# Performance work log

Hardware: AMD Instinct MI355X
Metric: run time of the kernel (lower is better)

The kernel has to match this reference:

```python
import jax, jax.numpy as jnp
import numpy as np
import math

B, S, IN = 16, 512, 8
D, H, L, FF, OUT = 512, 8, 4, 2048, 1
VAR_DIM = D // IN  # 64, even -> only sin/cos even-dim path in the original loop
HD = D // H
EPS = 1e-5


def setup_inputs() -> dict:
    key = jax.random.key(0)
    ks = jax.random.split(key, 20)
    s = 0.02
    inp = {
        "features": jax.random.normal(ks[0], (B, S, IN), dtype=jnp.float32),
        "position_indices": jax.random.randint(ks[1], (B, S), 0, 512, dtype=jnp.int64 if jax.config.jax_enable_x64 else jnp.int32),
        "w_in": jax.random.normal(ks[2], (IN, D), dtype=jnp.float32) * s,
        "b_in": jnp.zeros((D,), jnp.float32),
        "qkv_w": jax.random.normal(ks[3], (L, D, 3 * D), dtype=jnp.float32) * s,
        "qkv_b": jnp.zeros((L, 3 * D), jnp.float32),
        "attn_out_w": jax.random.normal(ks[4], (L, D, D), dtype=jnp.float32) * s,
        "attn_out_b": jnp.zeros((L, D), jnp.float32),
        "ln1_g": jnp.ones((L, D), jnp.float32),
        "ln1_b": jnp.zeros((L, D), jnp.float32),
        "ff1_w": jax.random.normal(ks[5], (L, D, FF), dtype=jnp.float32) * s,
        "ff1_b": jnp.zeros((L, FF), jnp.float32),
        "ff2_w": jax.random.normal(ks[6], (L, FF, D), dtype=jnp.float32) * s,
        "ff2_b": jnp.zeros((L, D), jnp.float32),
        "ln2_g": jnp.ones((L, D), jnp.float32),
        "ln2_b": jnp.zeros((L, D), jnp.float32),
        "w_out": jax.random.normal(ks[7], (D, OUT), dtype=jnp.float32) * s,
        "b_out": jnp.zeros((OUT,), jnp.float32),
    }
    return inp


def _pos_encoding(position_indices):
    # Vectorized replacement of the per-(b,i) Python loop.
    pos = position_indices.astype(jnp.float32)  # [B,S]
    div = jnp.exp(jnp.arange(0, VAR_DIM, 2, dtype=jnp.float32) * (-(math.log(10000.0) / VAR_DIM)))  # [VAR_DIM//2]
    ang = pos[:, :, None] * div  # [B,S,VAR_DIM//2]
    # interleave sin (even dims) / cos (odd dims) -> [B,S,VAR_DIM]
    block = jnp.stack([jnp.sin(ang), jnp.cos(ang)], axis=-1).reshape(pos.shape[0], pos.shape[1], VAR_DIM)
    # identical encoding per variable since var_positions == position_indices for all vars
    return jnp.tile(block, (1, 1, IN))  # [B,S,D]


def _layer_norm(x, g, b):
    mu = jnp.mean(x, axis=-1, keepdims=True)
    var = jnp.mean(jnp.square(x - mu), axis=-1, keepdims=True)
    return (x - mu) * jax.lax.rsqrt(var + EPS) * g + b


def _encoder_layer(x, qkv_w, qkv_b, ow, ob, g1, b1, f1w, f1b, f2w, f2b, g2, b2):
    Bx, Sx, _ = x.shape
    qkv = x @ qkv_w + qkv_b  # [B,S,3D]
    q, k, v = jnp.split(qkv, 3, axis=-1)
    q = q.reshape(Bx, Sx, H, HD)
    k = k.reshape(Bx, Sx, H, HD)
    v = v.reshape(Bx, Sx, H, HD)
    scores = jnp.einsum("bqhd,bkhd->bhqk", q, k) / math.sqrt(HD)
    attn = jax.nn.softmax(scores, axis=-1)
    ctx = jnp.einsum("bhqk,bkhd->bqhd", attn, v).reshape(Bx, Sx, D)
    attn_out = ctx @ ow + ob
    x = _layer_norm(x + attn_out, g1, b1)  # post-norm (PyTorch default norm_first=False)
    ff = jax.nn.relu(x @ f1w + f1b) @ f2w + f2b
    return _layer_norm(x + ff, g2, b2)


def reference(features, position_indices, w_in, b_in, qkv_w, qkv_b, attn_out_w, attn_out_b,
              ln1_g, ln1_b, ff1_w, ff1_b, ff2_w, ff2_b, ln2_g, ln2_b, w_out, b_out):
    x = features @ w_in + b_in  # input projection
    x = x + _pos_encoding(position_indices)
    for l in range(L):
        x = _encoder_layer(x, qkv_w[l], qkv_b[l], attn_out_w[l], attn_out_b[l],
                           ln1_g[l], ln1_b[l], ff1_w[l], ff1_b[l], ff2_w[l], ff2_b[l],
                           ln2_g[l], ln2_b[l])
    return x @ w_out + b_out  # [B,S,OUT]
```

## Files before the change

### kernel.cpp

```cpp
#include <hip/hip_runtime.h>
#include <cstdint>
#include <cstddef>

#define BATCH   16
#define SEQ     512
#define NTOK    8192
#define DMODEL  512
#define NHEAD   8
#define HDIM    64
#define FFDIM   2048
#define NLAYER  4

typedef unsigned short u16;
typedef __attribute__((ext_vector_type(8))) short bf16x8;
typedef __attribute__((ext_vector_type(8))) unsigned short us8;
typedef __attribute__((ext_vector_type(4))) float f32x4;

__device__ __forceinline__ float bf2f(u16 u) {
    union { float f; unsigned int i; } x; x.i = ((unsigned int)u) << 16; return x.f;
}
__device__ __forceinline__ u16 f2b(float f) {
    union { float f; unsigned int u; } a; a.f = f;
    unsigned int r = a.u + 0x7fff + ((a.u >> 16) & 1);
    return (u16)(r >> 16);
}

__device__ __forceinline__ void async_copy16(const void* g, void* l) {
    __builtin_amdgcn_global_load_lds(
        (const __attribute__((address_space(1))) unsigned int*)g,
        (__attribute__((address_space(3))) unsigned int*)l, 16, 0, 0);
}

__global__ __launch_bounds__(256) void embed_kernel(
    const float* __restrict__ feat, const int* __restrict__ pos,
    const float* __restrict__ w_in, const float* __restrict__ b_in,
    float* __restrict__ x, u16* __restrict__ xb)
{
    int idx = blockIdx.x * 256 + threadIdx.x;
    if (idx >= NTOK * DMODEL) return;
    int t = idx >> 9;
    int d = idx & 511;
    float acc = b_in[d];
#pragma unroll
    for (int i = 0; i < 8; ++i)
        acc += feat[t * 8 + i] * w_in[i * DMODEL + d];
    int p = pos[t];
    int dl = d & 63;
    int pair = dl >> 1;
    float div = expf(-(float)(2 * pair) * 0.14391156831212787f);
    float ang = (float)p * div;
    float pe = (dl & 1) ? cosf(ang) : sinf(ang);
    float v = acc + pe;
    x[idx] = v;
    xb[idx] = f2b(v);
}

__global__ __launch_bounds__(256) void transpose_w_kernel(
    const float* __restrict__ W, u16* __restrict__ WT, int K, int N)
{
    __shared__ float t[32][33];
    const float* Wl = W + (size_t)blockIdx.z * K * N;
    u16* WTl = WT + (size_t)blockIdx.z * K * N;
    int n0 = blockIdx.x * 32, k0 = blockIdx.y * 32;
    int c = threadIdx.x & 31, r8 = threadIdx.x >> 5;
#pragma unroll
    for (int i = 0; i < 4; ++i) {
        int r = r8 + i * 8;
        t[r][c] = Wl[(size_t)(k0 + r) * N + n0 + c];
    }
    __syncthreads();
#pragma unroll
    for (int i = 0; i < 4; ++i) {
        int r = r8 + i * 8;
        WTl[(size_t)(n0 + r) * K + k0 + c] = f2b(t[c][r]);
    }
}

template <int OUT_BF16, int RELU, int ADD_RESID>
__global__ __launch_bounds__(256) void gemm_bk64_kernel(
    const u16* __restrict__ A, const u16* __restrict__ BT,
    const float* __restrict__ bias, const float* __restrict__ resid,
    void* __restrict__ Cp, int M, int N, int K)
{
    __shared__ u16 As[128 * 64];
    __shared__ u16 Bs[128 * 64];
    const int tid = threadIdx.x;

    const int gx = gridDim.x, gy = gridDim.y;
    const int raw = blockIdx.x + gx * blockIdx.y;
    const int xcd = raw & 7;
    const int k8  = raw >> 3;
    const int ych = gy >> 3;
    const int m0 = (xcd * ych + k8 / gx) * 128;
    const int n0 = (k8 % gx) * 128;

    const int wid = tid >> 6, lane = tid & 63;
    const int wr = (wid >> 1) * 64, wc = (wid & 1) * 64;
    const int lr = lane & 15, lk16 = lane >> 4;
    const int sw = lr & 7;

    f32x4 acc[4][4] = {};

    for (int kt = 0; kt < K; kt += 64) {
        __syncthreads();
#pragma unroll
        for (int u = 0; u < 4; ++u) {
            int cc = u * 256 + tid;
            int row = cc >> 3, kc = cc & 7;
            async_copy16(&A[(size_t)(m0 + row) * K + kt + ((kc ^ (row & 7)) * 8)],
                         &As[cc * 8]);
        }
#pragma unroll
        for (int u = 0; u < 4; ++u) {
            int cc = u * 256 + tid;
            int row = cc >> 3, kc = cc & 7;
            async_copy16(&BT[(size_t)(n0 + row) * K + kt + ((kc ^ (row & 7)) * 8)],
                         &Bs[cc * 8]);
        }
        __syncthreads();

        bf16x8 a[4][2], b[4][2];
#pragma unroll
        for (int i = 0; i < 4; ++i)
#pragma unroll
            for (int kk = 0; kk < 2; ++kk) {
                a[i][kk] = *(const bf16x8*)&As[
                    (wr + i * 16 + lr) * 64 + (((kk * 4 + lk16) ^ sw) * 8)];
                b[i][kk] = *(const bf16x8*)&Bs[
                    (wc + i * 16 + lr) * 64 + (((kk * 4 + lk16) ^ sw) * 8)];
            }

        __builtin_amdgcn_s_setprio(1);
#pragma unroll
        for (int i = 0; i < 4; ++i)
#pragma unroll
            for (int j = 0; j < 4; ++j)
#pragma unroll
                for (int kk = 0; kk < 2; ++kk)
                    acc[i][j] = __builtin_amdgcn_mfma_f32_16x16x32_bf16(
                        a[i][kk], b[j][kk], acc[i][j], 0, 0, 0);
        __builtin_amdgcn_s_setprio(0);
    }

#pragma unroll
    for (int j = 0; j < 4; ++j) {
        int col = n0 + wc + j * 16 + lr;
        float bb = bias[col];
#pragma unroll
        for (int i = 0; i < 4; ++i) {
            int rbase = m0 + wr + i * 16 + lk16 * 4;
            f32x4 v = acc[i][j];
#pragma unroll
            for (int r = 0; r < 4; ++r) {
                float val = v[r] + bb;
                if (ADD_RESID) val += resid[(size_t)(rbase + r) * N + col];
                if (RELU) val = fmaxf(val, 0.f);
                if (OUT_BF16)
                    ((u16*)Cp)[(size_t)(rbase + r) * N + col] = f2b(val);
                else
                    ((float*)Cp)[(size_t)(rbase + r) * N + col] = val;
            }
        }
    }
}

__global__ __launch_bounds__(256) void attention_mfma_kernel(
    const u16* __restrict__ qkv, u16* __restrict__ ctx)
{
    __shared__ __align__(16) u16 Ks[2][64 * 64];
    __shared__ __align__(16) u16 Vt[64][72];
    __shared__ __align__(16) u16 Ps[4][16][72];

    const int tid = threadIdx.x;
    const int raw = blockIdx.x;
    const int xcd = raw & 7;
    const int k8  = raw >> 3;
    const int bh  = xcd * 16 + (k8 >> 3);
    const int b = bh >> 3, h = bh & 7;
    const int q0 = (k8 & 7) * 64;

    const int wid = tid >> 6, lane = tid & 63;
    const int lr = lane & 15;
    const int lk16 = lane >> 4;
    const size_t base = (size_t)b * SEQ * 1536;
    const int qrow = wid * 16 + lr;

    bf16x8 qf[2];
#pragma unroll
    for (int ks = 0; ks < 2; ++ks)
        qf[ks] = *(const bf16x8*)&qkv[base + (size_t)(q0 + qrow) * 1536 + h * 64
                                      + ks * 32 + lk16 * 8];

    const int vr0 = tid & 63;
    const int vc0 = (tid >> 6) * 8;
    const int vc1 = 32 + vc0;

#pragma unroll
    for (int j = 0; j < 2; ++j) {
        int c = j * 256 + tid;
        int row = c >> 3;
        int sc8 = ((c & 7) ^ (row & 7)) * 8;
        async_copy16(&qkv[base + (size_t)(row) * 1536 + 512 + h * 64 + sc8], &Ks[0][c * 8]);
    }
    us8 v0 = *(const us8*)&qkv[base + (size_t)(vr0) * 1536 + 1024 + h * 64 + vc0];
    us8 v1 = *(const us8*)&qkv[base + (size_t)(vr0) * 1536 + 1024 + h * 64 + vc1];
    __syncthreads();
#pragma unroll
    for (int e = 0; e < 8; ++e) { Vt[vc0 + e][vr0] = v0[e]; Vt[vc1 + e][vr0] = v1[e]; }
    __syncthreads();

    float l_r[4] = {0.f, 0.f, 0.f, 0.f};
    f32x4 o_acc[4] = {};

    for (int t = 0; t < SEQ / 64; ++t) {
        const int cur = t & 1;
        const bool more = (t + 1 < SEQ / 64);
        if (more) {
            const int kt1 = (t + 1) * 64;
#pragma unroll
            for (int j = 0; j < 2; ++j) {
                int c = j * 256 + tid;
                int row = c >> 3;
                int sc8 = ((c & 7) ^ (row & 7)) * 8;
                async_copy16(&qkv[base + (size_t)(kt1 + row) * 1536 + 512 + h * 64 + sc8],
                             &Ks[cur ^ 1][c * 8]);
            }
            v0 = *(const us8*)&qkv[base + (size_t)(kt1 + vr0) * 1536 + 1024 + h * 64 + vc0];
            v1 = *(const us8*)&qkv[base + (size_t)(kt1 + vr0) * 1536 + 1024 + h * 64 + vc1];
        }

        f32x4 sc[4] = {};
#pragma unroll
        for (int ks = 0; ks < 2; ++ks) {
#pragma unroll
            for (int j = 0; j < 4; ++j) {
                int krow = j * 16 + lr;
                bf16x8 bk = *(const bf16x8*)&Ks[cur][krow * 64 + ((ks * 4 + lk16) ^ (krow & 7)) * 8];
                sc[j] = __builtin_amdgcn_mfma_f32_16x16x32_bf16(qf[ks], bk, sc[j], 0, 0, 0);
            }
        }

        float pf[4][4];
#pragma unroll
        for (int r = 0; r < 4; ++r) {
            float s0 = 0.f;
#pragma unroll
            for (int j = 0; j < 4; ++j) {
                float p = __expf(sc[j][r] * 0.125f);
                pf[j][r] = p;
                s0 += p;
            }
#pragma unroll
            for (int m = 1; m < 16; m <<= 1)
                s0 += __shfl_xor(s0, m);
            l_r[r] += s0;
        }

#pragma unroll
        for (int j = 0; j < 4; ++j)
#pragma unroll
            for (int r = 0; r < 4; ++r)
                Ps[wid][lk16 * 4 + r][j * 16 + lr] = f2b(pf[j][r]);

#pragma unroll
        for (int kk = 0; kk < 2; ++kk) {
            bf16x8 ap = *(const bf16x8*)&Ps[wid][lr][kk * 32 + lk16 * 8];
#pragma unroll
            for (int j2 = 0; j2 < 4; ++j2) {
                bf16x8 bv = *(const bf16x8*)&Vt[j2 * 16 + lr][kk * 32 + lk16 * 8];
                o_acc[j2] = __builtin_amdgcn_mfma_f32_16x16x32_bf16(ap, bv, o_acc[j2], 0, 0, 0);
            }
        }

        __syncthreads();
        if (more) {
#pragma unroll
            for (int e = 0; e < 8; ++e) { Vt[vc0 + e][vr0] = v0[e]; Vt[vc1 + e][vr0] = v1[e]; }
        }
        __syncthreads();
    }

#pragma unroll
    for (int r = 0; r < 4; ++r) {
        float inv = 1.f / l_r[r];
        int t = b * SEQ + q0 + wid * 16 + lk16 * 4 + r;
        u16* op = &ctx[(size_t)t * DMODEL + h * 64];
#pragma unroll
        for (int j2 = 0; j2 < 4; ++j2)
            op[j2 * 16 + lr] = f2b(o_acc[j2][r] * inv);
    }
}

__global__ __launch_bounds__(256) void ln_kernel(
    const float* __restrict__ sum_in, float* __restrict__ x, u16* __restrict__ xb,
    const float* __restrict__ gamma, const float* __restrict__ beta)
{
    const int wave = threadIdx.x >> 6, lane = threadIdx.x & 63;
    const int t = blockIdx.x * 4 + wave;
    const float* sr = sum_in + (size_t)t * DMODEL;
    float* xr = x + (size_t)t * DMODEL;
    u16* xbr = xb + (size_t)t * DMODEL;

    float v[8];
    float sum = 0.f;
#pragma unroll
    for (int i = 0; i < 2; ++i) {
        float4 a = *reinterpret_cast<const float4*>(&sr[lane * 8 + i * 4]);
        v[i * 4 + 0] = a.x; v[i * 4 + 1] = a.y;
        v[i * 4 + 2] = a.z; v[i * 4 + 3] = a.w;
        sum += a.x + a.y + a.z + a.w;
    }
#pragma unroll
    for (int off = 32; off; off >>= 1) sum += __shfl_xor(sum, off);
    float mean = sum * (1.f / DMODEL);
    float vs = 0.f;
#pragma unroll
    for (int i = 0; i < 8; ++i) {
        float d = v[i] - mean;
        vs += d * d;
    }
#pragma unroll
    for (int off = 32; off; off >>= 1) vs += __shfl_xor(vs, off);
    float rstd = rsqrtf(vs * (1.f / DMODEL) + 1e-5f);
#pragma unroll
    for (int i = 0; i < 8; ++i) {
        int d = lane * 8 + i;
        float val = (v[i] - mean) * rstd * gamma[d] + beta[d];
        xr[d] = val;
        xbr[d] = f2b(val);
    }
}

__global__ __launch_bounds__(256) void out_kernel(
    const float* __restrict__ x, const float* __restrict__ w,
    const float* __restrict__ b, float* __restrict__ out)
{
    const int wave = threadIdx.x >> 6, lane = threadIdx.x & 63;
    const int t = blockIdx.x * 4 + wave;
    const float* xr = x + (size_t)t * DMODEL;
    float acc = 0.f;
#pragma unroll
    for (int i = 0; i < 2; ++i) {
        float4 a = *reinterpret_cast<const float4*>(&xr[lane * 8 + i * 4]);
        float4 ww = *reinterpret_cast<const float4*>(&w[lane * 8 + i * 4]);
        acc += a.x * ww.x + a.y * ww.y + a.z * ww.z + a.w * ww.w;
    }
#pragma unroll
    for (int off = 32; off; off >>= 1) acc += __shfl_xor(acc, off);
    if (lane == 0) out[t] = acc + b[0];
}

extern "C" void kernel_launch(void* const* d_in, const int* in_sizes, int n_in,
                              void* d_out, int out_size, void* d_ws, size_t ws_size,
                              hipStream_t stream)
{
    const float* features = (const float*)d_in[0];
    const int*   pos      = (const int*)  d_in[1];
    const float* w_in     = (const float*)d_in[2];
    const float* b_in     = (const float*)d_in[3];
    const float* qkv_w    = (const float*)d_in[4];
    const float* qkv_b    = (const float*)d_in[5];
    const float* ow       = (const float*)d_in[6];
    const float* ob       = (const float*)d_in[7];
    const float* g1       = (const float*)d_in[8];
    const float* b1       = (const float*)d_in[9];
    const float* ff1w     = (const float*)d_in[10];
    const float* ff1b     = (const float*)d_in[11];
    const float* ff2w     = (const float*)d_in[12];
    const float* ff2b     = (const float*)d_in[13];
    const float* g2       = (const float*)d_in[14];
    const float* b2       = (const float*)d_in[15];
    const float* w_out    = (const float*)d_in[16];
    const float* b_out    = (const float*)d_in[17];
    float* out = (float*)d_out;

    char* p = (char*)d_ws;
    auto alloc = [&](size_t bytes) { char* r = p; p += (bytes + 255) & ~(size_t)255; return r; };
    float* x   = (float*)alloc((size_t)NTOK * DMODEL * 4);
    u16*   xb  = (u16*)  alloc((size_t)NTOK * DMODEL * 2);
    u16*   big = (u16*)  alloc((size_t)NTOK * FFDIM * 2);
    u16*   ctx = (u16*)  alloc((size_t)NTOK * DMODEL * 2);
    float* tmp = (float*)alloc((size_t)NTOK * DMODEL * 4);
    u16* wqkvT = (u16*)alloc((size_t)NLAYER * DMODEL * 3 * DMODEL * 2);
    u16* owT   = (u16*)alloc((size_t)NLAYER * DMODEL * DMODEL * 2);
    u16* f1wT  = (u16*)alloc((size_t)NLAYER * DMODEL * FFDIM * 2);
    u16* f2wT  = (u16*)alloc((size_t)NLAYER * FFDIM * DMODEL * 2);

    transpose_w_kernel<<<dim3(3 * DMODEL / 32, DMODEL / 32, NLAYER), 256, 0, stream>>>(
        qkv_w, wqkvT, DMODEL, 3 * DMODEL);
    transpose_w_kernel<<<dim3(DMODEL / 32, DMODEL / 32, NLAYER), 256, 0, stream>>>(
        ow, owT, DMODEL, DMODEL);
    transpose_w_kernel<<<dim3(FFDIM / 32, DMODEL / 32, NLAYER), 256, 0, stream>>>(
        ff1w, f1wT, DMODEL, FFDIM);
    transpose_w_kernel<<<dim3(DMODEL / 32, FFDIM / 32, NLAYER), 256, 0, stream>>>(
        ff2w, f2wT, FFDIM, DMODEL);

    embed_kernel<<<(NTOK * DMODEL + 255) / 256, 256, 0, stream>>>(
        features, pos, w_in, b_in, x, xb);

    for (int l = 0; l < NLAYER; ++l) {
        gemm_bk64_kernel<1, 0, 0><<<dim3(3 * DMODEL / 128, NTOK / 128), 256, 0, stream>>>(
            xb, wqkvT + (size_t)l * DMODEL * 3 * DMODEL, qkv_b + (size_t)l * 3 * DMODEL,
            nullptr, big, NTOK, 3 * DMODEL, DMODEL);
        attention_mfma_kernel<<<BATCH * NHEAD * (SEQ / 64), 256, 0, stream>>>(big, ctx);
        gemm_bk64_kernel<0, 0, 1><<<dim3(DMODEL / 128, NTOK / 128), 256, 0, stream>>>(
            ctx, owT + (size_t)l * DMODEL * DMODEL, ob + (size_t)l * DMODEL, x,
            tmp, NTOK, DMODEL, DMODEL);
        ln_kernel<<<NTOK / 4, 256, 0, stream>>>(
            tmp, x, xb, g1 + (size_t)l * DMODEL, b1 + (size_t)l * DMODEL);
        gemm_bk64_kernel<1, 1, 0><<<dim3(FFDIM / 128, NTOK / 128), 256, 0, stream>>>(
            xb, f1wT + (size_t)l * DMODEL * FFDIM, ff1b + (size_t)l * FFDIM,
            nullptr, big, NTOK, FFDIM, DMODEL);
        gemm_bk64_kernel<0, 0, 1><<<dim3(DMODEL / 128, NTOK / 128), 256, 0, stream>>>(
            big, f2wT + (size_t)l * FFDIM * DMODEL, ff2b + (size_t)l * DMODEL, x,
            tmp, NTOK, DMODEL, FFDIM);
        ln_kernel<<<NTOK / 4, 256, 0, stream>>>(
            tmp, x, xb, g2 + (size_t)l * DMODEL, b2 + (size_t)l * DMODEL);
    }

    out_kernel<<<NTOK / 4, 256, 0, stream>>>(x, w_out, b_out, out);
}
```

Baseline: 668.2 us.

## Double-buffer LDS tiles in bf16 GEMM to overlap loads with MFMA

```diff
diff --git a/kernel.cpp b/kernel.cpp
--- a/kernel.cpp
+++ b/kernel.cpp
@@ -82,8 +82,8 @@
     const float* __restrict__ bias, const float* __restrict__ resid,
     void* __restrict__ Cp, int M, int N, int K)
 {
-    __shared__ u16 As[128 * 64];
-    __shared__ u16 Bs[128 * 64];
+    __shared__ u16 As[2][128 * 64];
+    __shared__ u16 Bs[2][128 * 64];
     const int tid = threadIdx.x;
 
     const int gx = gridDim.x, gy = gridDim.y;
@@ -100,33 +100,41 @@
     const int sw = lr & 7;
 
     f32x4 acc[4][4] = {};
-
-    for (int kt = 0; kt < K; kt += 64) {
-        __syncthreads();
-#pragma unroll
-        for (int u = 0; u < 4; ++u) {
-            int cc = u * 256 + tid;
-            int row = cc >> 3, kc = cc & 7;
-            async_copy16(&A[(size_t)(m0 + row) * K + kt + ((kc ^ (row & 7)) * 8)],
-                         &As[cc * 8]);
-        }
-#pragma unroll
-        for (int u = 0; u < 4; ++u) {
-            int cc = u * 256 + tid;
-            int row = cc >> 3, kc = cc & 7;
-            async_copy16(&BT[(size_t)(n0 + row) * K + kt + ((kc ^ (row & 7)) * 8)],
-                         &Bs[cc * 8]);
-        }
-        __syncthreads();
+    const int T = K >> 6;
+
+#define STAGE_TILE(buf, kt)                                                    \
+    {                                                                          \
+        _Pragma("unroll")                                                      \
+        for (int u = 0; u < 4; ++u) {                                          \
+            int cc = u * 256 + tid;                                            \
+            int row = cc >> 3, kc = cc & 7;                                    \
+            async_copy16(&A[(size_t)(m0 + row) * K + (kt) + ((kc ^ (row & 7)) * 8)], \
+                         &As[buf][cc * 8]);                                    \
+        }                                                                      \
+        _Pragma("unroll")                                                      \
+        for (int u = 0; u < 4; ++u) {                                          \
+            int cc = u * 256 + tid;                                            \
+            int row = cc >> 3, kc = cc & 7;                                    \
+            async_copy16(&BT[(size_t)(n0 + row) * K + (kt) + ((kc ^ (row & 7)) * 8)], \
+                         &Bs[buf][cc * 8]);                                    \
+        }                                                                      \
+    }
+
+    STAGE_TILE(0, 0);
+    __syncthreads();
+
+    for (int t = 0; t < T; ++t) {
+        const int cur = t & 1;
+        if (t + 1 < T) STAGE_TILE(cur ^ 1, (t + 1) * 64);
 
         bf16x8 a[4][2], b[4][2];
 #pragma unroll
         for (int i = 0; i < 4; ++i)
 #pragma unroll
             for (int kk = 0; kk < 2; ++kk) {
-                a[i][kk] = *(const bf16x8*)&As[
+                a[i][kk] = *(const bf16x8*)&As[cur][
                     (wr + i * 16 + lr) * 64 + (((kk * 4 + lk16) ^ sw) * 8)];
-                b[i][kk] = *(const bf16x8*)&Bs[
+                b[i][kk] = *(const bf16x8*)&Bs[cur][
                     (wc + i * 16 + lr) * 64 + (((kk * 4 + lk16) ^ sw) * 8)];
             }
 
@@ -140,7 +148,10 @@
                     acc[i][j] = __builtin_amdgcn_mfma_f32_16x16x32_bf16(
                         a[i][kk], b[j][kk], acc[i][j], 0, 0, 0);
         __builtin_amdgcn_s_setprio(0);
-    }
+
+        __syncthreads();
+    }
+#undef STAGE_TILE
 
 #pragma unroll
     for (int j = 0; j < 4; ++j) {
```

New measurement: 678.0 us. No clear change (+1.5%).
